# Optimization experiments

Measured on AMD Instinct MI355X. Metric: run time of the kernel, lower is better.

Reference implementation:

```python
import jax, jax.numpy as jnp
import numpy as np

DIM = 384
NUM_HEADS = 12
WINDOW = (8, 8)
HEAD_DIM = DIM // NUM_HEADS
CPB_HIDDEN = 512
MAX_LOGIT = float(np.log(1.0 / 0.01))  # clamp for logit_scale


def _relative_coords_table(ws):
    # log-spaced continuous relative coordinate table (Swin V2 style), ND
    axes = [np.arange(-(w - 1), w, dtype=np.float32) for w in ws]
    grid = np.stack(np.meshgrid(*axes, indexing='ij'), axis=-1)
    grid = grid.reshape(-1, len(ws))  # (prod(2w-1), nd)
    for i, w in enumerate(ws):
        grid[:, i] /= max(w - 1, 1)
    grid *= 8.0
    grid = np.sign(grid) * np.log2(np.abs(grid) + 1.0) / np.log2(8.0)
    return grid.astype(np.float32)


def _relative_position_index(ws):
    coords = np.stack(np.meshgrid(*[np.arange(w) for w in ws], indexing='ij'), axis=0)
    coords = coords.reshape(len(ws), -1)  # (nd, N)
    rel = coords[:, :, None] - coords[:, None, :]  # (nd, N, N)
    rel = rel.transpose(1, 2, 0).astype(np.int64)  # (N, N, nd)
    for i, w in enumerate(ws):
        rel[..., i] += w - 1
    # row-major strides over table dims of size (2w-1)
    stride = 1
    for i in range(len(ws) - 1, -1, -1):
        rel[..., i] *= stride
        stride *= 2 * ws[i] - 1
    return rel.sum(-1).astype(np.int32)  # (N, N)


def setup_inputs() -> dict:
    key = jax.random.key(0)
    ks = jax.random.split(key, 8)
    B, N = 1024, int(np.prod(WINDOW))
    x = jax.random.normal(ks[0], (B, N, DIM), dtype=jnp.float32)
    mask = jax.random.normal(ks[1], (64, N, N), dtype=jnp.float32)
    qkv_w = jax.random.normal(ks[2], (DIM, 3 * DIM), dtype=jnp.float32) * (DIM ** -0.5)
    proj_w = jax.random.normal(ks[3], (DIM, DIM), dtype=jnp.float32) * (DIM ** -0.5)
    proj_b = jnp.zeros((DIM,), dtype=jnp.float32)
    cpb_w1 = jax.random.normal(ks[4], (len(WINDOW), CPB_HIDDEN), dtype=jnp.float32) * 0.5
    cpb_b1 = jnp.zeros((CPB_HIDDEN,), dtype=jnp.float32)
    cpb_w2 = jax.random.normal(ks[5], (CPB_HIDDEN, NUM_HEADS), dtype=jnp.float32) * (CPB_HIDDEN ** -0.5)
    cpb_b2 = jnp.zeros((NUM_HEADS,), dtype=jnp.float32)
    logit_scale = jnp.log(jnp.ones((NUM_HEADS, 1, 1), dtype=jnp.float32) * 10.0)
    rpb_table = jnp.asarray(_relative_coords_table(WINDOW))
    rpb_idx = jnp.asarray(_relative_position_index(WINDOW))
    return dict(x=x, mask=mask, qkv_w=qkv_w, proj_w=proj_w, proj_b=proj_b,
                cpb_w1=cpb_w1, cpb_b1=cpb_b1, cpb_w2=cpb_w2, cpb_b2=cpb_b2,
                logit_scale=logit_scale, rpb_table=rpb_table, rpb_idx=rpb_idx)


def reference(x, mask, qkv_w, proj_w, proj_b, cpb_w1, cpb_b1, cpb_w2, cpb_b2,
              logit_scale, rpb_table, rpb_idx):
    B, N, _ = x.shape
    qkv = (x @ qkv_w).reshape(B, N, 3, NUM_HEADS, HEAD_DIM)
    qkv = qkv.transpose(2, 0, 3, 1, 4)  # (3, B, H, N, D)
    q, k, v = qkv[0], qkv[1], qkv[2]

    def _normalize(t):
        norm_sq = jnp.sum(t * t, axis=-1, keepdims=True)
        return t * jax.lax.rsqrt(jnp.maximum(norm_sq, 1e-12))

    q = _normalize(q)
    k = _normalize(k)
    attn = jnp.einsum('bhqd,bhkd->bhqk', q, k)
    scale = jnp.exp(jnp.minimum(logit_scale, MAX_LOGIT))  # (H,1,1)
    attn = attn * scale

    # continuous relative position bias MLP: Dense(512)+relu -> Dense(H)
    rpb = jax.nn.relu(rpb_table @ cpb_w1 + cpb_b1) @ cpb_w2 + cpb_b2  # (T, H)
    rpb = jnp.take(rpb, rpb_idx.reshape(-1), axis=0).reshape(N, N, NUM_HEADS)
    rpb = jnp.transpose(rpb, (2, 0, 1))  # (H, N, N)
    attn = attn + 16.0 * jax.nn.sigmoid(rpb)[None]

    n_w = mask.shape[0]
    attn = attn.reshape(B // n_w, n_w, NUM_HEADS, N, N)
    attn = attn + mask[None, :, None, :, :]
    attn = attn.reshape(B, NUM_HEADS, N, N)

    attn = jax.nn.softmax(attn, axis=-1)
    out = jnp.einsum('bhqk,bhkd->bhqd', attn, v)
    out = out.transpose(0, 2, 1, 3).reshape(B, N, DIM)
    return out @ proj_w + proj_b
```

## Files before the change

### kernel.cpp

```cpp
#include <hip/hip_runtime.h>

typedef unsigned short u16;
typedef __attribute__((ext_vector_type(8))) short short8;
typedef __attribute__((ext_vector_type(4))) float f32x4;

#define MFMA16(a, b, c) __builtin_amdgcn_mfma_f32_16x16x32_bf16((a), (b), (c), 0, 0, 0)

#define OFF_BIAS 0
#define OFF_SCALES 196608
#define OFF_RPB 196672
#define OFF_QKVF 207616
#define OFF_PROJF 1092352
#define OFF_XF 1387264
#define WS_NEED (1387264UL + 50331648UL)


__device__ __forceinline__ u16 f2bf(float f) {
  unsigned x = __float_as_uint(f);
  return (u16)((x + 0x7fffu + ((x >> 16) & 1u)) >> 16);
}

__global__ __launch_bounds__(256) void prep_cpb(const float* __restrict__ tab, const float* __restrict__ w1,
                                                const float* __restrict__ b1, const float* __restrict__ w2,
                                                const float* __restrict__ b2, float* __restrict__ rpb) {
  const int t = blockIdx.x;
  const int tid = threadIdx.x;
  const float t0 = tab[2 * t], t1 = tab[2 * t + 1];
  float acc[12];
#pragma unroll
  for (int h = 0; h < 12; ++h) acc[h] = 0.f;
  for (int j = tid; j < 512; j += 256) {
    const float hv = fmaxf(t0 * w1[j] + t1 * w1[512 + j] + b1[j], 0.f);
#pragma unroll
    for (int h = 0; h < 12; ++h) acc[h] += hv * w2[j * 12 + h];
  }
#pragma unroll
  for (int h = 0; h < 12; ++h)
#pragma unroll
    for (int off = 1; off < 64; off <<= 1) acc[h] += __shfl_xor(acc[h], off);
  __shared__ float red[4][12];
  const int wave = tid >> 6;
  if ((tid & 63) == 0) {
#pragma unroll
    for (int h = 0; h < 12; ++h) red[wave][h] = acc[h];
  }
  __syncthreads();
  if (tid < 12) rpb[t * 12 + tid] = red[0][tid] + red[1][tid] + red[2][tid] + red[3][tid] + b2[tid];
}

__global__ __launch_bounds__(256) void prep_all(const float* __restrict__ x,
                                                const float* __restrict__ qkv_w,
                                                const float* __restrict__ proj_w,
                                                const float* __restrict__ logit_scale,
                                                const float* __restrict__ rpb,
                                                const int* __restrict__ rpb_idx,
                                                u16* __restrict__ xF, u16* __restrict__ qkvF,
                                                u16* __restrict__ projF, float* __restrict__ scales,
                                                float* __restrict__ bias, int bid0) {
  __shared__ __align__(16) u16 sm[24576];
  const int bid = blockIdx.x + bid0;
  const int tid = threadIdx.x;
  if (bid < 1024) {
    const float4* x4 = reinterpret_cast<const float4*>(x + (long)bid * 24576);
#pragma unroll
    for (int it = 0; it < 12; ++it) {
      const int c = it * 256 + tid;
      const float4 a = x4[2 * c];
      const float4 b = x4[2 * c + 1];
      short8 v;
      v[0] = (short)f2bf(a.x); v[1] = (short)f2bf(a.y); v[2] = (short)f2bf(a.z); v[3] = (short)f2bf(a.w);
      v[4] = (short)f2bf(b.x); v[5] = (short)f2bf(b.y); v[6] = (short)f2bf(b.z); v[7] = (short)f2bf(b.w);
      const int row = c / 48;
      *reinterpret_cast<short8*>(sm + ((c * 8) ^ ((row & 7) << 3))) = v;
    }
    __syncthreads();
    u16* dst = xF + (long)bid * 24576;
#pragma unroll
    for (int it = 0; it < 12; ++it) {
      const int slot = it * 256 + tid;
      const int f = slot >> 6, l = slot & 63;
      const int row = 16 * (f & 3) + (l & 15);
      const int k0 = (f >> 2) * 32 + (l >> 4) * 8;
      const short8 v = *reinterpret_cast<const short8*>(sm + ((row * 384 + k0) ^ ((row & 7) << 3)));
      *reinterpret_cast<short8*>(dst + slot * 8) = v;
    }
  } else if (bid < 1168) {
    u16(*tile)[66] = reinterpret_cast<u16(*)[66]>(sm);
    const float* src;
    int W, rt, ct;
    const bool isqkv = bid < 1132;
    if (isqkv) {
      const int b = bid - 1024;
      src = qkv_w; W = 1152; rt = b / 18; ct = b % 18;
    } else {
      const int b = bid - 1132;
      src = proj_w; W = 384; rt = b / 6; ct = b % 6;
    }
#pragma unroll
    for (int kk = 0; kk < 4; ++kk) {
      const int idx = tid + kk * 256;
      const int r = idx >> 4, c4 = idx & 15;
      const float4 v = *reinterpret_cast<const float4*>(src + (long)(rt * 64 + r) * W + ct * 64 + c4 * 4);
      tile[r][c4 * 4 + 0] = f2bf(v.x);
      tile[r][c4 * 4 + 1] = f2bf(v.y);
      tile[r][c4 * 4 + 2] = f2bf(v.z);
      tile[r][c4 * 4 + 3] = f2bf(v.w);
    }
    __syncthreads();
#pragma unroll
    for (int kk = 0; kk < 4; ++kk) {
      const int idx = tid + kk * 256;
      const int c = idx >> 4, r0 = (idx & 15) * 4;
      ushort4 o;
      o.x = tile[r0 + 0][c];
      o.y = tile[r0 + 1][c];
      o.z = tile[r0 + 2][c];
      o.w = tile[r0 + 3][c];
      const int col = ct * 64 + c, k = rt * 64 + r0;
      const int lane = ((k >> 3) & 3) * 16 + (col & 15);
      const int e = k & 7;
      long off;
      if (isqkv) {
        const int m = col / 384, colm = col - m * 384;
        const int h = colm >> 5, jn = (colm >> 4) & 1;
        off = (long)(((h * 3 + m) * 24) + (k >> 5) * 2 + jn) * 512 + lane * 8 + e;
        *reinterpret_cast<ushort4*>(qkvF + off) = o;
      } else {
        const int w = col / 96, colw = col - w * 96;
        const int jn = colw >> 4;
        off = (long)(w * 72 + (k >> 5) * 6 + jn) * 512 + lane * 8 + e;
        *reinterpret_cast<ushort4*>(projF + off) = o;
      }
    }
  } else if (bid == 1168) {
    if (tid < 12) scales[tid] = __expf(fminf(logit_scale[tid], 4.6051702f));
  } else {
    const int p = (bid - 1169) * 256 + tid;
    const int t = rpb_idx[p];
#pragma unroll
    for (int h = 0; h < 12; ++h) bias[h * 4096 + p] = 16.f / (1.f + __expf(-rpb[t * 12 + h]));
  }
}

__global__ __launch_bounds__(768) void attn_fused(const u16* __restrict__ xF,
                                                  const float* __restrict__ mask,
                                                  const u16* __restrict__ qkvF,
                                                  const float* __restrict__ scales,
                                                  const float* __restrict__ bias,
                                                  const u16* __restrict__ projF,
                                                  const float* __restrict__ proj_b,
                                                  float* __restrict__ out) {
  __shared__ __align__(16) u16 sm[73728];
  const int tid = threadIdx.x;
  const int wave = tid >> 6, lane = tid & 63;
  const int q16 = lane >> 4, c16 = lane & 15;
  const int widx = blockIdx.x, wm = widx & 63;
  const int h = wave;
  u16* qs = sm + wave * 6144;
  u16* ks = qs + 2048;
  u16* ps = qs;
  u16* vst = qs + 4096;
  const u16* xw = xF + (long)widx * 24576;
  const u16* hb = qkvF + (long)h * 72 * 512;
  const float sc = scales[h];
  const f32x4 fzero = {0.f, 0.f, 0.f, 0.f};

  {
    f32x4 qa[4][2], ka[4][2];
#pragma unroll
    for (int i = 0; i < 4; ++i)
#pragma unroll
      for (int j = 0; j < 2; ++j) {
        qa[i][j] = fzero; ka[i][j] = fzero;
      }
#pragma unroll 1
    for (int t = 0; t < 12; ++t) {
      short8 af[4];
#pragma unroll
      for (int i = 0; i < 4; ++i)
        af[i] = *reinterpret_cast<const short8*>(xw + ((t * 4 + i) * 64 + lane) * 8);
#pragma unroll
      for (int jn = 0; jn < 2; ++jn) {
        const int fi = (2 * t + jn) * 512 + lane * 8;
        const short8 bq = *reinterpret_cast<const short8*>(hb + fi);
        const short8 bk = *reinterpret_cast<const short8*>(hb + 24 * 512 + fi);
#pragma unroll
        for (int i = 0; i < 4; ++i) {
          qa[i][jn] = MFMA16(af[i], bq, qa[i][jn]);
          ka[i][jn] = MFMA16(af[i], bk, ka[i][jn]);
        }
      }
    }
#pragma unroll
    for (int i = 0; i < 4; ++i) {
#pragma unroll
      for (int r = 0; r < 4; ++r) {
        const int row = 16 * i + 4 * q16 + r;
        float sq = qa[i][0][r] * qa[i][0][r] + qa[i][1][r] * qa[i][1][r];
        float sk = ka[i][0][r] * ka[i][0][r] + ka[i][1][r] * ka[i][1][r];
#pragma unroll
        for (int off = 1; off < 16; off <<= 1) {
          sq += __shfl_xor(sq, off);
          sk += __shfl_xor(sk, off);
        }
        const float rq = rsqrtf(fmaxf(sq, 1e-12f)) * sc;
        const float rk = rsqrtf(fmaxf(sk, 1e-12f));
        const int swq = (row & 3) << 3;
#pragma unroll
        for (int jn = 0; jn < 2; ++jn) {
          const int col = 16 * jn + c16;
          qs[(row * 32 + col) ^ swq] = f2bf(qa[i][jn][r] * rq);
          ks[(row * 32 + col) ^ swq] = f2bf(ka[i][jn][r] * rk);
        }
      }
    }
  }
  __builtin_amdgcn_sched_barrier(0);
  {
    f32x4 va[4][2];
#pragma unroll
    for (int i = 0; i < 4; ++i) {
      va[i][0] = fzero;
      va[i][1] = fzero;
    }
#pragma unroll 1
    for (int t = 0; t < 12; ++t) {
      short8 af[4];
#pragma unroll
      for (int i = 0; i < 4; ++i)
        af[i] = *reinterpret_cast<const short8*>(xw + ((t * 4 + i) * 64 + lane) * 8);
#pragma unroll
      for (int jn = 0; jn < 2; ++jn) {
        const short8 bv = *reinterpret_cast<const short8*>(hb + 48 * 512 + (2 * t + jn) * 512 + lane * 8);
#pragma unroll
        for (int i = 0; i < 4; ++i) va[i][jn] = MFMA16(af[i], bv, va[i][jn]);
      }
    }
#pragma unroll
    for (int i = 0; i < 4; ++i)
#pragma unroll
      for (int jn = 0; jn < 2; ++jn) {
        const int d = 16 * jn + c16;
        ushort4 vv;
        vv.x = f2bf(va[i][jn][0]);
        vv.y = f2bf(va[i][jn][1]);
        vv.z = f2bf(va[i][jn][2]);
        vv.w = f2bf(va[i][jn][3]);
        *reinterpret_cast<ushort4*>(vst + ((d * 64 + 16 * i + 4 * q16) ^ ((d & 7) << 3))) = vv;
      }
  }
  __builtin_amdgcn_sched_barrier(0);
  short8 aq[4], bk4[4];
#pragma unroll
  for (int i = 0; i < 4; ++i) {
    const int row = c16 + 16 * i;
    aq[i] = *reinterpret_cast<const short8*>(qs + ((row * 32 + q16 * 8) ^ ((row & 3) << 3)));
    bk4[i] = *reinterpret_cast<const short8*>(ks + ((row * 32 + q16 * 8) ^ ((row & 3) << 3)));
  }
  __builtin_amdgcn_sched_barrier(0);
  const float* bh = bias + h * 4096;
  const float* mw = mask + (long)wm * 4096;
#pragma unroll
  for (int i = 0; i < 4; ++i) {
    f32x4 si[4];
#pragma unroll
    for (int j = 0; j < 4; ++j) {
      const int col = 16 * j + c16;
#pragma unroll
      for (int r = 0; r < 4; ++r) {
        const int row = 16 * i + 4 * q16 + r;
        si[j][r] = bh[row * 64 + col] + mw[row * 64 + col];
      }
    }
#pragma unroll
    for (int j = 0; j < 4; ++j) si[j] = MFMA16(aq[i], bk4[j], si[j]);
#pragma unroll
    for (int r = 0; r < 4; ++r) {
      float m = fmaxf(fmaxf(si[0][r], si[1][r]), fmaxf(si[2][r], si[3][r]));
#pragma unroll
      for (int off = 1; off < 16; off <<= 1) m = fmaxf(m, __shfl_xor(m, off));
      float e[4], s = 0.f;
#pragma unroll
      for (int j = 0; j < 4; ++j) {
        e[j] = __expf(si[j][r] - m);
        s += e[j];
      }
#pragma unroll
      for (int off = 1; off < 16; off <<= 1) s += __shfl_xor(s, off);
      const float inv = 1.f / s;
      const int row = 16 * i + 4 * q16 + r;
      const int sw = (row & 7) << 3;
#pragma unroll
      for (int j = 0; j < 4; ++j) ps[(row * 64 + 16 * j + c16) ^ sw] = f2bf(e[j] * inv);
    }
    f32x4 oi[2];
    oi[0] = fzero;
    oi[1] = fzero;
    const int rowp = c16 + 16 * i;
#pragma unroll
    for (int kt = 0; kt < 2; ++kt) {
      const short8 api = *reinterpret_cast<const short8*>(
          ps + ((rowp * 64 + kt * 32 + q16 * 8) ^ ((rowp & 7) << 3)));
#pragma unroll
      for (int jn = 0; jn < 2; ++jn) {
        const int d = 16 * jn + c16;
        const short8 bvf = *reinterpret_cast<const short8*>(
            vst + ((d * 64 + kt * 32 + q16 * 8) ^ ((d & 7) << 3)));
        oi[jn] = MFMA16(api, bvf, oi[jn]);
      }
    }
#pragma unroll
    for (int jn = 0; jn < 2; ++jn)
#pragma unroll
      for (int r = 0; r < 4; ++r) {
        const int row = 16 * i + 4 * q16 + r;
        qs[(row * 32 + 16 * jn + c16) ^ ((row & 3) << 3)] = f2bf(oi[jn][r]);
      }
    __builtin_amdgcn_sched_barrier(0);
  }
  __syncthreads();
  const int n16a = wave * 2, n16b = wave * 2 + 1;
  const u16* pba = projF + (long)((n16a / 6) * 72 + (n16a % 6)) * 512;
  const u16* pbb = projF + (long)((n16b / 6) * 72 + (n16b % 6)) * 512;
  f32x4 pacc[4][2];
#pragma unroll
  for (int i = 0; i < 4; ++i) {
    pacc[i][0] = fzero;
    pacc[i][1] = fzero;
  }
#pragma unroll 1
  for (int t = 0; t < 12; ++t) {
    const u16* reg = sm + t * 6144;
    short8 af[4];
#pragma unroll
    for (int i = 0; i < 4; ++i) {
      const int row = c16 + 16 * i;
      af[i] = *reinterpret_cast<const short8*>(reg + ((row * 32 + q16 * 8) ^ ((row & 3) << 3)));
    }
    const short8 bwa = *reinterpret_cast<const short8*>(pba + (long)t * 6 * 512 + lane * 8);
    const short8 bwb = *reinterpret_cast<const short8*>(pbb + (long)t * 6 * 512 + lane * 8);
#pragma unroll
    for (int i = 0; i < 4; ++i) {
      pacc[i][0] = MFMA16(af[i], bwa, pacc[i][0]);
      pacc[i][1] = MFMA16(af[i], bwb, pacc[i][1]);
    }
  }
  float* ob = out + (long)widx * 24576;
#pragma unroll
  for (int jnp = 0; jnp < 2; ++jnp) {
    const int n = (wave * 2 + jnp) * 16 + c16;
    const float bv = proj_b[n];
#pragma unroll
    for (int i = 0; i < 4; ++i)
#pragma unroll
      for (int r = 0; r < 4; ++r)
        ob[(long)(16 * i + 4 * q16 + r) * 384 + n] = pacc[i][jnp][r] + bv;
  }
}

__global__ __launch_bounds__(256, 1) void attn_fb(const float* __restrict__ x,
                                                  const float* __restrict__ mask,
                                                  const u16* __restrict__ qkvF,
                                                  const float* __restrict__ scales,
                                                  const float* __restrict__ bias,
                                                  const u16* __restrict__ projF,
                                                  const float* __restrict__ proj_b,
                                                  float* __restrict__ out) {
  __shared__ __align__(16) u16 sm[49152];
  const int tid = threadIdx.x;
  const int wave = tid >> 6, lane = tid & 63;
  const int q16 = lane >> 4, c16 = lane & 15;
  const int widx = blockIdx.x, wm = widx & 63;
  u16* qs = sm + wave * 6144;
  u16* ks = qs + 2048;
  u16* ps = qs;
  u16* vst = qs + 4096;
  u16* xs = sm + 24576;
  const f32x4 fzero = {0.f, 0.f, 0.f, 0.f};
  {
    const float4* x4 = reinterpret_cast<const float4*>(x + (long)widx * 24576);
#pragma unroll
    for (int it = 0; it < 12; ++it) {
      const int c = it * 256 + tid;
      const float4 a = x4[2 * c];
      const float4 b = x4[2 * c + 1];
      short8 v;
      v[0] = (short)f2bf(a.x); v[1] = (short)f2bf(a.y); v[2] = (short)f2bf(a.z); v[3] = (short)f2bf(a.w);
      v[4] = (short)f2bf(b.x); v[5] = (short)f2bf(b.y); v[6] = (short)f2bf(b.z); v[7] = (short)f2bf(b.w);
      const int row = c / 48;
      *reinterpret_cast<short8*>(xs + ((c * 8) ^ ((row & 7) << 3))) = v;
    }
  }
  __syncthreads();
  unsigned ow[3][4][2][2];
#pragma unroll
  for (int hh = 0; hh < 3; ++hh) {
    const int h = wave * 3 + hh;
    const float sc = scales[h];
    const u16* hb = qkvF + (long)h * 72 * 512;
    f32x4 qa[4][2], ka[4][2], va[4][2];
#pragma unroll
    for (int i = 0; i < 4; ++i)
#pragma unroll
      for (int j = 0; j < 2; ++j) {
        qa[i][j] = fzero; ka[i][j] = fzero; va[i][j] = fzero;
      }
#pragma unroll 1
    for (int t = 0; t < 12; ++t) {
      const int k0 = t * 32 + q16 * 8;
      short8 af[4];
#pragma unroll
      for (int i = 0; i < 4; ++i) {
        const int row = c16 + 16 * i;
        af[i] = *reinterpret_cast<const short8*>(xs + ((row * 384 + k0) ^ ((row & 7) << 3)));
      }
#pragma unroll
      for (int jn = 0; jn < 2; ++jn) {
        const int fi = (2 * t + jn) * 512 + lane * 8;
        const short8 bq = *reinterpret_cast<const short8*>(hb + fi);
        const short8 bk = *reinterpret_cast<const short8*>(hb + 24 * 512 + fi);
        const short8 bv = *reinterpret_cast<const short8*>(hb + 48 * 512 + fi);
#pragma unroll
        for (int i = 0; i < 4; ++i) {
          qa[i][jn] = MFMA16(af[i], bq, qa[i][jn]);
          ka[i][jn] = MFMA16(af[i], bk, ka[i][jn]);
          va[i][jn] = MFMA16(af[i], bv, va[i][jn]);
        }
      }
    }
#pragma unroll
    for (int i = 0; i < 4; ++i) {
#pragma unroll
      for (int r = 0; r < 4; ++r) {
        const int row = 16 * i + 4 * q16 + r;
        float sq = qa[i][0][r] * qa[i][0][r] + qa[i][1][r] * qa[i][1][r];
        float sk = ka[i][0][r] * ka[i][0][r] + ka[i][1][r] * ka[i][1][r];
#pragma unroll
        for (int off = 1; off < 16; off <<= 1) {
          sq += __shfl_xor(sq, off);
          sk += __shfl_xor(sk, off);
        }
        const float rq = rsqrtf(fmaxf(sq, 1e-12f)) * sc;
        const float rk = rsqrtf(fmaxf(sk, 1e-12f));
        const int swq = (row & 3) << 3;
#pragma unroll
        for (int jn = 0; jn < 2; ++jn) {
          const int col = 16 * jn + c16;
          qs[(row * 32 + col) ^ swq] = f2bf(qa[i][jn][r] * rq);
          ks[(row * 32 + col) ^ swq] = f2bf(ka[i][jn][r] * rk);
          vst[(col * 64 + row) ^ ((col & 7) << 3)] = f2bf(va[i][jn][r]);
        }
      }
    }
    f32x4 sacc[4][4];
    {
      const float* bh = bias + h * 4096;
      const float* mw = mask + (long)wm * 4096;
#pragma unroll
      for (int i = 0; i < 4; ++i)
#pragma unroll
        for (int j = 0; j < 4; ++j) {
          const int col = 16 * j + c16;
#pragma unroll
          for (int r = 0; r < 4; ++r) {
            const int row = 16 * i + 4 * q16 + r;
            sacc[i][j][r] = bh[row * 64 + col] + mw[row * 64 + col];
          }
        }
    }
    short8 aq[4], bk4[4];
#pragma unroll
    for (int i = 0; i < 4; ++i) {
      const int row = c16 + 16 * i;
      aq[i] = *reinterpret_cast<const short8*>(qs + ((row * 32 + q16 * 8) ^ ((row & 3) << 3)));
      bk4[i] = *reinterpret_cast<const short8*>(ks + ((row * 32 + q16 * 8) ^ ((row & 3) << 3)));
    }
#pragma unroll
    for (int i = 0; i < 4; ++i)
#pragma unroll
      for (int j = 0; j < 4; ++j) sacc[i][j] = MFMA16(aq[i], bk4[j], sacc[i][j]);
#pragma unroll
    for (int i = 0; i < 4; ++i) {
#pragma unroll
      for (int r = 0; r < 4; ++r) {
        float m = fmaxf(fmaxf(sacc[i][0][r], sacc[i][1][r]), fmaxf(sacc[i][2][r], sacc[i][3][r]));
#pragma unroll
        for (int off = 1; off < 16; off <<= 1) m = fmaxf(m, __shfl_xor(m, off));
        float e[4], s = 0.f;
#pragma unroll
        for (int j = 0; j < 4; ++j) {
          e[j] = __expf(sacc[i][j][r] - m);
          s += e[j];
        }
#pragma unroll
        for (int off = 1; off < 16; off <<= 1) s += __shfl_xor(s, off);
        const float inv = 1.f / s;
        const int row = 16 * i + 4 * q16 + r;
        const int sw = (row & 7) << 3;
#pragma unroll
        for (int j = 0; j < 4; ++j) ps[(row * 64 + 16 * j + c16) ^ sw] = f2bf(e[j] * inv);
      }
    }
    f32x4 oa[4][2];
#pragma unroll
    for (int i = 0; i < 4; ++i) {
      oa[i][0] = fzero;
      oa[i][1] = fzero;
    }
#pragma unroll
    for (int kt = 0; kt < 2; ++kt) {
      short8 ap[4], bv2[2];
#pragma unroll
      for (int i = 0; i < 4; ++i) {
        const int row = c16 + 16 * i;
        ap[i] = *reinterpret_cast<const short8*>(ps + ((row * 64 + kt * 32 + q16 * 8) ^ ((row & 7) << 3)));
      }
#pragma unroll
      for (int jn = 0; jn < 2; ++jn) {
        const int d = 16 * jn + c16;
        bv2[jn] = *reinterpret_cast<const short8*>(vst + ((d * 64 + kt * 32 + q16 * 8) ^ ((d & 7) << 3)));
      }
#pragma unroll
      for (int i = 0; i < 4; ++i)
#pragma unroll
        for (int jn = 0; jn < 2; ++jn) oa[i][jn] = MFMA16(ap[i], bv2[jn], oa[i][jn]);
    }
#pragma unroll
    for (int i = 0; i < 4; ++i)
#pragma unroll
      for (int jn = 0; jn < 2; ++jn) {
        ow[hh][i][jn][0] = (unsigned)f2bf(oa[i][jn][0]) | ((unsigned)f2bf(oa[i][jn][1]) << 16);
        ow[hh][i][jn][1] = (unsigned)f2bf(oa[i][jn][2]) | ((unsigned)f2bf(oa[i][jn][3]) << 16);
      }
  }
  __syncthreads();
#pragma unroll
  for (int hh = 0; hh < 3; ++hh) {
    const int cb = (wave * 3 + hh) * 32;
#pragma unroll
    for (int i = 0; i < 4; ++i)
#pragma unroll
      for (int jn = 0; jn < 2; ++jn)
#pragma unroll
        for (int p = 0; p < 2; ++p) {
          const unsigned w = ow[hh][i][jn][p];
          const int col = cb + 16 * jn + c16;
          const int r0 = 16 * i + 4 * q16 + 2 * p;
          xs[(r0 * 384 + col) ^ ((r0 & 7) << 3)] = (u16)(w & 0xffffu);
          xs[((r0 + 1) * 384 + col) ^ (((r0 + 1) & 7) << 3)] = (u16)(w >> 16);
        }
  }
  __syncthreads();
  const u16* pb = projF + (long)wave * 72 * 512;
  f32x4 pacc[4][6];
#pragma unroll
  for (int i = 0; i < 4; ++i)
#pragma unroll
    for (int jn = 0; jn < 6; ++jn) pacc[i][jn] = fzero;
#pragma unroll 1
  for (int t = 0; t < 12; ++t) {
    const int k0 = t * 32 + q16 * 8;
    short8 af[4];
#pragma unroll
    for (int i = 0; i < 4; ++i) {
      const int row = c16 + 16 * i;
      af[i] = *reinterpret_cast<const short8*>(xs + ((row * 384 + k0) ^ ((row & 7) << 3)));
    }
#pragma unroll
    for (int jn = 0; jn < 6; ++jn) {
      const short8 bw = *reinterpret_cast<const short8*>(pb + (t * 6 + jn) * 512 + lane * 8);
#pragma unroll
      for (int i = 0; i < 4; ++i) pacc[i][jn] = MFMA16(af[i], bw, pacc[i][jn]);
    }
  }
  float* ob = out + (long)widx * 24576;
#pragma unroll
  for (int jn = 0; jn < 6; ++jn) {
    const int n = wave * 96 + 16 * jn + c16;
    const float bv = proj_b[n];
#pragma unroll
    for (int i = 0; i < 4; ++i)
#pragma unroll
      for (int r = 0; r < 4; ++r)
        ob[(long)(16 * i + 4 * q16 + r) * 384 + n] = pacc[i][jn][r] + bv;
  }
}

extern "C" void kernel_launch(void* const* d_in, const int* in_sizes, int n_in, void* d_out,
                              int out_size, void* d_ws, size_t ws_size, hipStream_t stream) {
  const float* x = (const float*)d_in[0];
  const float* mask = (const float*)d_in[1];
  const float* qkv_w = (const float*)d_in[2];
  const float* proj_w = (const float*)d_in[3];
  const float* proj_b = (const float*)d_in[4];
  const float* cpb_w1 = (const float*)d_in[5];
  const float* cpb_b1 = (const float*)d_in[6];
  const float* cpb_w2 = (const float*)d_in[7];
  const float* cpb_b2 = (const float*)d_in[8];
  const float* logit_scale = (const float*)d_in[9];
  const float* rpb_table = (const float*)d_in[10];
  const int* rpb_idx = (const int*)d_in[11];

  char* ws = (char*)d_ws;
  float* bias = (float*)(ws + OFF_BIAS);
  float* scales = (float*)(ws + OFF_SCALES);
  float* rpb = (float*)(ws + OFF_RPB);
  u16* qkvF = (u16*)(ws + OFF_QKVF);
  u16* projF = (u16*)(ws + OFF_PROJF);
  u16* xF = (u16*)(ws + OFF_XF);

  prep_cpb<<<225, 256, 0, stream>>>(rpb_table, cpb_w1, cpb_b1, cpb_w2, cpb_b2, rpb);
  const bool big = ws_size >= WS_NEED;
  if (big) {
    prep_all<<<1185, 256, 0, stream>>>(x, qkv_w, proj_w, logit_scale, rpb, rpb_idx,
                                       xF, qkvF, projF, scales, bias, 0);
    attn_fused<<<1024, 768, 0, stream>>>(xF, mask, qkvF, scales, bias, projF, proj_b,
                                         (float*)d_out);
  } else {
    prep_all<<<161, 256, 0, stream>>>(x, qkv_w, proj_w, logit_scale, rpb, rpb_idx,
                                      xF, qkvF, projF, scales, bias, 1024);
    attn_fb<<<1024, 256, 0, stream>>>(x, mask, qkvF, scales, bias, projF, proj_b, (float*)d_out);
  }
}
```

Baseline: 343.7 us.

## Fuse CPB MLP into prep kernel and gather sigmoid bias in attention

Removes the separate prep_cpb launch by folding the per-table-entry position-bias MLP into extra blocks of prep_all, which now stores the 16*sigmoid bias per table entry (225x12) instead of a full 12x64x64 expanded bias. The attention kernels gather the bias through rpb_idx at use time. This saves one launch and the expanded bias write, at the cost of an indirect, dependent load per score element. The fallback attention kernel is also rewritten to use 768 threads with one head per wave, matching the fused path.

```diff
diff --git a/kernel.cpp b/kernel.cpp
--- a/kernel.cpp
+++ b/kernel.cpp
@@ -6,9 +6,8 @@
 
 #define MFMA16(a, b, c) __builtin_amdgcn_mfma_f32_16x16x32_bf16((a), (b), (c), 0, 0, 0)
 
-#define OFF_BIAS 0
-#define OFF_SCALES 196608
-#define OFF_RPB 196672
+#define OFF_SIG 0
+#define OFF_SCALES 16384
 #define OFF_QKVF 207616
 #define OFF_PROJF 1092352
 #define OFF_XF 1387264
@@ -20,43 +19,18 @@
   return (u16)((x + 0x7fffu + ((x >> 16) & 1u)) >> 16);
 }
 
-__global__ __launch_bounds__(256) void prep_cpb(const float* __restrict__ tab, const float* __restrict__ w1,
-                                                const float* __restrict__ b1, const float* __restrict__ w2,
-                                                const float* __restrict__ b2, float* __restrict__ rpb) {
-  const int t = blockIdx.x;
-  const int tid = threadIdx.x;
-  const float t0 = tab[2 * t], t1 = tab[2 * t + 1];
-  float acc[12];
-#pragma unroll
-  for (int h = 0; h < 12; ++h) acc[h] = 0.f;
-  for (int j = tid; j < 512; j += 256) {
-    const float hv = fmaxf(t0 * w1[j] + t1 * w1[512 + j] + b1[j], 0.f);
-#pragma unroll
-    for (int h = 0; h < 12; ++h) acc[h] += hv * w2[j * 12 + h];
-  }
-#pragma unroll
-  for (int h = 0; h < 12; ++h)
-#pragma unroll
-    for (int off = 1; off < 64; off <<= 1) acc[h] += __shfl_xor(acc[h], off);
-  __shared__ float red[4][12];
-  const int wave = tid >> 6;
-  if ((tid & 63) == 0) {
-#pragma unroll
-    for (int h = 0; h < 12; ++h) red[wave][h] = acc[h];
-  }
-  __syncthreads();
-  if (tid < 12) rpb[t * 12 + tid] = red[0][tid] + red[1][tid] + red[2][tid] + red[3][tid] + b2[tid];
-}
-
 __global__ __launch_bounds__(256) void prep_all(const float* __restrict__ x,
                                                 const float* __restrict__ qkv_w,
                                                 const float* __restrict__ proj_w,
                                                 const float* __restrict__ logit_scale,
-                                                const float* __restrict__ rpb,
-                                                const int* __restrict__ rpb_idx,
+                                                const float* __restrict__ tab,
+                                                const float* __restrict__ w1,
+                                                const float* __restrict__ b1,
+                                                const float* __restrict__ w2,
+                                                const float* __restrict__ b2,
                                                 u16* __restrict__ xF, u16* __restrict__ qkvF,
                                                 u16* __restrict__ projF, float* __restrict__ scales,
-                                                float* __restrict__ bias, int bid0) {
+                                                float* __restrict__ sig, int bid0) {
   __shared__ __align__(16) u16 sm[24576];
   const int bid = blockIdx.x + bid0;
   const int tid = threadIdx.x;
@@ -135,10 +109,31 @@
   } else if (bid == 1168) {
     if (tid < 12) scales[tid] = __expf(fminf(logit_scale[tid], 4.6051702f));
   } else {
-    const int p = (bid - 1169) * 256 + tid;
-    const int t = rpb_idx[p];
-#pragma unroll
-    for (int h = 0; h < 12; ++h) bias[h * 4096 + p] = 16.f / (1.f + __expf(-rpb[t * 12 + h]));
+    const int t = bid - 1169;
+    const float t0 = tab[2 * t], t1 = tab[2 * t + 1];
+    float acc[12];
+#pragma unroll
+    for (int h = 0; h < 12; ++h) acc[h] = 0.f;
+    for (int j = tid; j < 512; j += 256) {
+      const float hv = fmaxf(t0 * w1[j] + t1 * w1[512 + j] + b1[j], 0.f);
+#pragma unroll
+      for (int h = 0; h < 12; ++h) acc[h] += hv * w2[j * 12 + h];
+    }
+#pragma unroll
+    for (int h = 0; h < 12; ++h)
+#pragma unroll
+      for (int off = 1; off < 64; off <<= 1) acc[h] += __shfl_xor(acc[h], off);
+    float* red = reinterpret_cast<float*>(sm);
+    const int wave = tid >> 6;
+    if ((tid & 63) == 0) {
+#pragma unroll
+      for (int h = 0; h < 12; ++h) red[wave * 12 + h] = acc[h];
+    }
+    __syncthreads();
+    if (tid < 12) {
+      const float v = red[tid] + red[12 + tid] + red[24 + tid] + red[36 + tid] + b2[tid];
+      sig[t * 12 + tid] = 16.f / (1.f + __expf(-v));
+    }
   }
 }
 
@@ -146,7 +141,8 @@
                                                   const float* __restrict__ mask,
                                                   const u16* __restrict__ qkvF,
                                                   const float* __restrict__ scales,
-                                                  const float* __restrict__ bias,
+                                                  const int* __restrict__ rpb_idx,
+                                                  const float* __restrict__ sig,
                                                   const u16* __restrict__ projF,
                                                   const float* __restrict__ proj_b,
                                                   float* __restrict__ out) {
@@ -258,7 +254,6 @@
     bk4[i] = *reinterpret_cast<const short8*>(ks + ((row * 32 + q16 * 8) ^ ((row & 3) << 3)));
   }
   __builtin_amdgcn_sched_barrier(0);
-  const float* bh = bias + h * 4096;
   const float* mw = mask + (long)wm * 4096;
 #pragma unroll
   for (int i = 0; i < 4; ++i) {
@@ -269,7 +264,8 @@
 #pragma unroll
       for (int r = 0; r < 4; ++r) {
         const int row = 16 * i + 4 * q16 + r;
-        si[j][r] = bh[row * 64 + col] + mw[row * 64 + col];
+        const int p = row * 64 + col;
+        si[j][r] = sig[rpb_idx[p] * 12 + h] + mw[p];
       }
     }
 #pragma unroll
@@ -358,73 +354,69 @@
   }
 }
 
-__global__ __launch_bounds__(256, 1) void attn_fb(const float* __restrict__ x,
-                                                  const float* __restrict__ mask,
-                                                  const u16* __restrict__ qkvF,
-                                                  const float* __restrict__ scales,
-                                                  const float* __restrict__ bias,
-                                                  const u16* __restrict__ projF,
-                                                  const float* __restrict__ proj_b,
-                                                  float* __restrict__ out) {
-  __shared__ __align__(16) u16 sm[49152];
+__global__ __launch_bounds__(768) void attn_fb(const float* __restrict__ x,
+                                               const float* __restrict__ mask,
+                                               const u16* __restrict__ qkvF,
+                                               const float* __restrict__ scales,
+                                               const int* __restrict__ rpb_idx,
+                                               const float* __restrict__ sig,
+                                               const u16* __restrict__ projF,
+                                               const float* __restrict__ proj_b,
+                                               float* __restrict__ out) {
+  __shared__ __align__(16) u16 sm[73728];
+  u16* xs = sm;
   const int tid = threadIdx.x;
   const int wave = tid >> 6, lane = tid & 63;
   const int q16 = lane >> 4, c16 = lane & 15;
   const int widx = blockIdx.x, wm = widx & 63;
-  u16* qs = sm + wave * 6144;
-  u16* ks = qs + 2048;
-  u16* ps = qs;
-  u16* vst = qs + 4096;
-  u16* xs = sm + 24576;
-  const f32x4 fzero = {0.f, 0.f, 0.f, 0.f};
+  const int h = wave;
   {
-    const float4* x4 = reinterpret_cast<const float4*>(x + (long)widx * 24576);
-#pragma unroll
-    for (int it = 0; it < 12; ++it) {
-      const int c = it * 256 + tid;
-      const float4 a = x4[2 * c];
-      const float4 b = x4[2 * c + 1];
+    const float* xwf = x + (long)widx * 24576;
+#pragma unroll
+    for (int it = 0; it < 4; ++it) {
+      const int slot = it * 768 + tid;
+      const int f = slot >> 6, l = slot & 63;
+      const int row = 16 * (f & 3) + (l & 15);
+      const int k0 = (f >> 2) * 32 + (l >> 4) * 8;
+      const float4 a = *reinterpret_cast<const float4*>(xwf + row * 384 + k0);
+      const float4 b = *reinterpret_cast<const float4*>(xwf + row * 384 + k0 + 4);
       short8 v;
       v[0] = (short)f2bf(a.x); v[1] = (short)f2bf(a.y); v[2] = (short)f2bf(a.z); v[3] = (short)f2bf(a.w);
       v[4] = (short)f2bf(b.x); v[5] = (short)f2bf(b.y); v[6] = (short)f2bf(b.z); v[7] = (short)f2bf(b.w);
-      const int row = c / 48;
-      *reinterpret_cast<short8*>(xs + ((c * 8) ^ ((row & 7) << 3))) = v;
+      *reinterpret_cast<short8*>(xs + slot * 8) = v;
     }
   }
   __syncthreads();
-  unsigned ow[3][4][2][2];
-#pragma unroll
-  for (int hh = 0; hh < 3; ++hh) {
-    const int h = wave * 3 + hh;
-    const float sc = scales[h];
-    const u16* hb = qkvF + (long)h * 72 * 512;
-    f32x4 qa[4][2], ka[4][2], va[4][2];
+  u16* qs = sm + 24576 + wave * 4096;
+  u16* ks = qs + 2048;
+  u16* ps = qs;
+  const u16* hb = qkvF + (long)h * 72 * 512;
+  const float sc = scales[h];
+  const f32x4 fzero = {0.f, 0.f, 0.f, 0.f};
+  f32x4 va[4][2];
+  {
+    f32x4 qa[4][2], ka[4][2];
 #pragma unroll
     for (int i = 0; i < 4; ++i)
 #pragma unroll
       for (int j = 0; j < 2; ++j) {
-        qa[i][j] = fzero; ka[i][j] = fzero; va[i][j] = fzero;
+        qa[i][j] = fzero; ka[i][j] = fzero;
       }
 #pragma unroll 1
     for (int t = 0; t < 12; ++t) {
-      const int k0 = t * 32 + q16 * 8;
       short8 af[4];
 #pragma unroll
-      for (int i = 0; i < 4; ++i) {
-        const int row = c16 + 16 * i;
-        af[i] = *reinterpret_cast<const short8*>(xs + ((row * 384 + k0) ^ ((row & 7) << 3)));
-      }
+      for (int i = 0; i < 4; ++i)
+        af[i] = *reinterpret_cast<const short8*>(xs + ((t * 4 + i) * 64 + lane) * 8);
 #pragma unroll
       for (int jn = 0; jn < 2; ++jn) {
         const int fi = (2 * t + jn) * 512 + lane * 8;
         const short8 bq = *reinterpret_cast<const short8*>(hb + fi);
         const short8 bk = *reinterpret_cast<const short8*>(hb + 24 * 512 + fi);
-        const short8 bv = *reinterpret_cast<const short8*>(hb + 48 * 512 + fi);
 #pragma unroll
         for (int i = 0; i < 4; ++i) {
           qa[i][jn] = MFMA16(af[i], bq, qa[i][jn]);
           ka[i][jn] = MFMA16(af[i], bk, ka[i][jn]);
-          va[i][jn] = MFMA16(af[i], bv, va[i][jn]);
         }
       }
     }
@@ -448,141 +440,160 @@
           const int col = 16 * jn + c16;
           qs[(row * 32 + col) ^ swq] = f2bf(qa[i][jn][r] * rq);
           ks[(row * 32 + col) ^ swq] = f2bf(ka[i][jn][r] * rk);
-          vst[(col * 64 + row) ^ ((col & 7) << 3)] = f2bf(va[i][jn][r]);
         }
       }
     }
-    f32x4 sacc[4][4];
-    {
-      const float* bh = bias + h * 4096;
-      const float* mw = mask + (long)wm * 4096;
-#pragma unroll
-      for (int i = 0; i < 4; ++i)
-#pragma unroll
-        for (int j = 0; j < 4; ++j) {
-          const int col = 16 * j + c16;
-#pragma unroll
-          for (int r = 0; r < 4; ++r) {
-            const int row = 16 * i + 4 * q16 + r;
-            sacc[i][j][r] = bh[row * 64 + col] + mw[row * 64 + col];
-          }
-        }
-    }
-    short8 aq[4], bk4[4];
-#pragma unroll
-    for (int i = 0; i < 4; ++i) {
-      const int row = c16 + 16 * i;
-      aq[i] = *reinterpret_cast<const short8*>(qs + ((row * 32 + q16 * 8) ^ ((row & 3) << 3)));
-      bk4[i] = *reinterpret_cast<const short8*>(ks + ((row * 32 + q16 * 8) ^ ((row & 3) << 3)));
-    }
-#pragma unroll
-    for (int i = 0; i < 4; ++i)
-#pragma unroll
-      for (int j = 0; j < 4; ++j) sacc[i][j] = MFMA16(aq[i], bk4[j], sacc[i][j]);
-#pragma unroll
-    for (int i = 0; i < 4; ++i) {
-#pragma unroll
-      for (int r = 0; r < 4; ++r) {
-        float m = fmaxf(fmaxf(sacc[i][0][r], sacc[i][1][r]), fmaxf(sacc[i][2][r], sacc[i][3][r]));
-#pragma unroll
-        for (int off = 1; off < 16; off <<= 1) m = fmaxf(m, __shfl_xor(m, off));
-        float e[4], s = 0.f;
-#pragma unroll
-        for (int j = 0; j < 4; ++j) {
-          e[j] = __expf(sacc[i][j][r] - m);
-          s += e[j];
-        }
-#pragma unroll
-        for (int off = 1; off < 16; off <<= 1) s += __shfl_xor(s, off);
-        const float inv = 1.f / s;
-        const int row = 16 * i + 4 * q16 + r;
-        const int sw = (row & 7) << 3;
-#pragma unroll
-        for (int j = 0; j < 4; ++j) ps[(row * 64 + 16 * j + c16) ^ sw] = f2bf(e[j] * inv);
-      }
-    }
-    f32x4 oa[4][2];
-#pragma unroll
-    for (int i = 0; i < 4; ++i) {
-      oa[i][0] = fzero;
-      oa[i][1] = fzero;
-    }
-#pragma unroll
-    for (int kt = 0; kt < 2; ++kt) {
-      short8 ap[4], bv2[2];
-#pragma unroll
-      for (int i = 0; i < 4; ++i) {
-        const int row = c16 + 16 * i;
-        ap[i] = *reinterpret_cast<const short8*>(ps + ((row * 64 + kt * 32 + q16 * 8) ^ ((row & 7) << 3)));
-      }
-#pragma unroll
-      for (int jn = 0; jn < 2; ++jn) {
-        const int d = 16 * jn + c16;
-        bv2[jn] = *reinterpret_cast<const short8*>(vst + ((d * 64 + kt * 32 + q16 * 8) ^ ((d & 7) << 3)));
-      }
-#pragma unroll
-      for (int i = 0; i < 4; ++i)
-#pragma unroll
-        for (int jn = 0; jn < 2; ++jn) oa[i][jn] = MFMA16(ap[i], bv2[jn], oa[i][jn]);
-    }
-#pragma unroll
-    for (int i = 0; i < 4; ++i)
-#pragma unroll
-      for (int jn = 0; jn < 2; ++jn) {
-        ow[hh][i][jn][0] = (unsigned)f2bf(oa[i][jn][0]) | ((unsigned)f2bf(oa[i][jn][1]) << 16);
-        ow[hh][i][jn][1] = (unsigned)f2bf(oa[i][jn][2]) | ((unsigned)f2bf(oa[i][jn][3]) << 16);
-      }
-  }
-  __syncthreads();
-#pragma unroll
-  for (int hh = 0; hh < 3; ++hh) {
-    const int cb = (wave * 3 + hh) * 32;
-#pragma unroll
-    for (int i = 0; i < 4; ++i)
-#pragma unroll
-      for (int jn = 0; jn < 2; ++jn)
-#pragma unroll
-        for (int p = 0; p < 2; ++p) {
-          const unsigned w = ow[hh][i][jn][p];
-          const int col = cb + 16 * jn + c16;
-          const int r0 = 16 * i + 4 * q16 + 2 * p;
-          xs[(r0 * 384 + col) ^ ((r0 & 7) << 3)] = (u16)(w & 0xffffu);
-          xs[((r0 + 1) * 384 + col) ^ (((r0 + 1) & 7) << 3)] = (u16)(w >> 16);
-        }
-  }
-  __syncthreads();
-  const u16* pb = projF + (long)wave * 72 * 512;
-  f32x4 pacc[4][6];
-#pragma unroll
-  for (int i = 0; i < 4; ++i)
-#pragma unroll
-    for (int jn = 0; jn < 6; ++jn) pacc[i][jn] = fzero;
+  }
+#pragma unroll
+  for (int i = 0; i < 4; ++i) {
+    va[i][0] = fzero;
+    va[i][1] = fzero;
+  }
 #pragma unroll 1
   for (int t = 0; t < 12; ++t) {
-    const int k0 = t * 32 + q16 * 8;
     short8 af[4];
 #pragma unroll
+    for (int i = 0; i < 4; ++i)
+      af[i] = *reinterpret_cast<const short8*>(xs + ((t * 4 + i) * 64 + lane) * 8);
+#pragma unroll
+    for (int jn = 0; jn < 2; ++jn) {
+      const short8 bv = *reinterpret_cast<const short8*>(hb + 48 * 512 + (2 * t + jn) * 512 + lane * 8);
+#pragma unroll
+      for (int i = 0; i < 4; ++i) va[i][jn] = MFMA16(af[i], bv, va[i][jn]);
+    }
+  }
+  short8 aq[4], bk4[4];
+#pragma unroll
+  for (int i = 0; i < 4; ++i) {
+    const int row = c16 + 16 * i;
+    aq[i] = *reinterpret_cast<const short8*>(qs + ((row * 32 + q16 * 8) ^ ((row & 3) << 3)));
+    bk4[i] = *reinterpret_cast<const short8*>(ks + ((row * 32 + q16 * 8) ^ ((row & 3) << 3)));
+  }
+  const float* mw = mask + (long)wm * 4096;
+  f32x4 sacc[4][4];
+#pragma unroll
+  for (int i = 0; i < 4; ++i)
+#pragma unroll
+    for (int j = 0; j < 4; ++j) {
+      const int col = 16 * j + c16;
+#pragma unroll
+      for (int r = 0; r < 4; ++r) {
+        const int p = (16 * i + 4 * q16 + r) * 64 + col;
+        sacc[i][j][r] = sig[rpb_idx[p] * 12 + h] + mw[p];
+      }
+    }
+#pragma unroll
+  for (int i = 0; i < 4; ++i)
+#pragma unroll
+    for (int j = 0; j < 4; ++j) sacc[i][j] = MFMA16(aq[i], bk4[j], sacc[i][j]);
+#pragma unroll
+  for (int i = 0; i < 4; ++i)
+#pragma unroll
+    for (int r = 0; r < 4; ++r) {
+      float m = fmaxf(fmaxf(sacc[i][0][r], sacc[i][1][r]), fmaxf(sacc[i][2][r], sacc[i][3][r]));
+#pragma unroll
+      for (int off = 1; off < 16; off <<= 1) m = fmaxf(m, __shfl_xor(m, off));
+      float e[4], s = 0.f;
+#pragma unroll
+      for (int j = 0; j < 4; ++j) {
+        e[j] = __expf(sacc[i][j][r] - m);
+        s += e[j];
+      }
+#pragma unroll
+      for (int off = 1; off < 16; off <<= 1) s += __shfl_xor(s, off);
+      const float inv = 1.f / s;
+      const int row = 16 * i + 4 * q16 + r;
+      const int sw = (row & 7) << 3;
+#pragma unroll
+      for (int j = 0; j < 4; ++j) ps[(row * 64 + 16 * j + c16) ^ sw] = f2bf(e[j] * inv);
+    }
+  __syncthreads();
+  u16* vstb = sm + wave * 4096;
+#pragma unroll
+  for (int i = 0; i < 4; ++i)
+#pragma unroll
+    for (int jn = 0; jn < 2; ++jn) {
+      const int d = 16 * jn + c16;
+      ushort4 vv;
+      vv.x = f2bf(va[i][jn][0]);
+      vv.y = f2bf(va[i][jn][1]);
+      vv.z = f2bf(va[i][jn][2]);
+      vv.w = f2bf(va[i][jn][3]);
+      *reinterpret_cast<ushort4*>(vstb + ((d * 64 + 16 * i + 4 * q16) ^ ((d & 7) << 3))) = vv;
+    }
+  f32x4 oa[4][2];
+#pragma unroll
+  for (int i = 0; i < 4; ++i) {
+    oa[i][0] = fzero;
+    oa[i][1] = fzero;
+  }
+#pragma unroll
+  for (int kt = 0; kt < 2; ++kt) {
+    short8 ap[4], bv2[2];
+#pragma unroll
     for (int i = 0; i < 4; ++i) {
       const int row = c16 + 16 * i;
-      af[i] = *reinterpret_cast<const short8*>(xs + ((row * 384 + k0) ^ ((row & 7) << 3)));
-    }
-#pragma unroll
-    for (int jn = 0; jn < 6; ++jn) {
-      const short8 bw = *reinterpret_cast<const short8*>(pb + (t * 6 + jn) * 512 + lane * 8);
-#pragma unroll
-      for (int i = 0; i < 4; ++i) pacc[i][jn] = MFMA16(af[i], bw, pacc[i][jn]);
+      ap[i] = *reinterpret_cast<const short8*>(ps + ((row * 64 + kt * 32 + q16 * 8) ^ ((row & 7) << 3)));
+    }
+#pragma unroll
+    for (int jn = 0; jn < 2; ++jn) {
+      const int d = 16 * jn + c16;
+      bv2[jn] = *reinterpret_cast<const short8*>(vstb + ((d * 64 + kt * 32 + q16 * 8) ^ ((d & 7) << 3)));
+    }
+#pragma unroll
+    for (int i = 0; i < 4; ++i)
+#pragma unroll
+      for (int jn = 0; jn < 2; ++jn) oa[i][jn] = MFMA16(ap[i], bv2[jn], oa[i][jn]);
+  }
+  __syncthreads();
+  u16* ot = sm + 24576 + wave * 2048;
+  ot = sm + wave * 4096;
+#pragma unroll
+  for (int i = 0; i < 4; ++i)
+#pragma unroll
+    for (int jn = 0; jn < 2; ++jn)
+#pragma unroll
+      for (int r = 0; r < 4; ++r) {
+        const int row = 16 * i + 4 * q16 + r;
+        ot[(row * 32 + 16 * jn + c16) ^ ((row & 3) << 3)] = f2bf(oa[i][jn][r]);
+      }
+  __syncthreads();
+  const int n16a = wave * 2, n16b = wave * 2 + 1;
+  const u16* pba = projF + (long)((n16a / 6) * 72 + (n16a % 6)) * 512;
+  const u16* pbb = projF + (long)((n16b / 6) * 72 + (n16b % 6)) * 512;
+  f32x4 pacc[4][2];
+#pragma unroll
+  for (int i = 0; i < 4; ++i) {
+    pacc[i][0] = fzero;
+    pacc[i][1] = fzero;
+  }
+#pragma unroll 1
+  for (int t = 0; t < 12; ++t) {
+    const u16* reg = sm + t * 4096;
+    short8 af[4];
+#pragma unroll
+    for (int i = 0; i < 4; ++i) {
+      const int row = c16 + 16 * i;
+      af[i] = *reinterpret_cast<const short8*>(reg + ((row * 32 + q16 * 8) ^ ((row & 3) << 3)));
+    }
+    const short8 bwa = *reinterpret_cast<const short8*>(pba + (long)t * 6 * 512 + lane * 8);
+    const short8 bwb = *reinterpret_cast<const short8*>(pbb + (long)t * 6 * 512 + lane * 8);
+#pragma unroll
+    for (int i = 0; i < 4; ++i) {
+      pacc[i][0] = MFMA16(af[i], bwa, pacc[i][0]);
+      pacc[i][1] = MFMA16(af[i], bwb, pacc[i][1]);
     }
   }
   float* ob = out + (long)widx * 24576;
 #pragma unroll
-  for (int jn = 0; jn < 6; ++jn) {
-    const int n = wave * 96 + 16 * jn + c16;
+  for (int jnp = 0; jnp < 2; ++jnp) {
+    const int n = (wave * 2 + jnp) * 16 + c16;
     const float bv = proj_b[n];
 #pragma unroll
     for (int i = 0; i < 4; ++i)
 #pragma unroll
       for (int r = 0; r < 4; ++r)
-        ob[(long)(16 * i + 4 * q16 + r) * 384 + n] = pacc[i][jn][r] + bv;
+        ob[(long)(16 * i + 4 * q16 + r) * 384 + n] = pacc[i][jnp][r] + bv;
   }
 }
 
@@ -602,23 +613,22 @@
   const int* rpb_idx = (const int*)d_in[11];
 
   char* ws = (char*)d_ws;
-  float* bias = (float*)(ws + OFF_BIAS);
+  float* sig = (float*)(ws + OFF_SIG);
   float* scales = (float*)(ws + OFF_SCALES);
-  float* rpb = (float*)(ws + OFF_RPB);
   u16* qkvF = (u16*)(ws + OFF_QKVF);
   u16* projF = (u16*)(ws + OFF_PROJF);
   u16* xF = (u16*)(ws + OFF_XF);
 
-  prep_cpb<<<225, 256, 0, stream>>>(rpb_table, cpb_w1, cpb_b1, cpb_w2, cpb_b2, rpb);
   const bool big = ws_size >= WS_NEED;
   if (big) {
-    prep_all<<<1185, 256, 0, stream>>>(x, qkv_w, proj_w, logit_scale, rpb, rpb_idx,
-                                       xF, qkvF, projF, scales, bias, 0);
-    attn_fused<<<1024, 768, 0, stream>>>(xF, mask, qkvF, scales, bias, projF, proj_b,
+    prep_all<<<1394, 256, 0, stream>>>(x, qkv_w, proj_w, logit_scale, rpb_table, cpb_w1,
+                                       cpb_b1, cpb_w2, cpb_b2, xF, qkvF, projF, scales, sig, 0);
+    attn_fused<<<1024, 768, 0, stream>>>(xF, mask, qkvF, scales, rpb_idx, sig, projF, proj_b,
                                          (float*)d_out);
   } else {
-    prep_all<<<161, 256, 0, stream>>>(x, qkv_w, proj_w, logit_scale, rpb, rpb_idx,
-                                      xF, qkvF, projF, scales, bias, 1024);
-    attn_fb<<<1024, 256, 0, stream>>>(x, mask, qkvF, scales, bias, projF, proj_b, (float*)d_out);
+    prep_all<<<370, 256, 0, stream>>>(x, qkv_w, proj_w, logit_scale, rpb_table, cpb_w1,
+                                      cpb_b1, cpb_w2, cpb_b2, xF, qkvF, projF, scales, sig, 1024);
+    attn_fb<<<1024, 768, 0, stream>>>(x, mask, qkvF, scales, rpb_idx, sig, projF, proj_b,
+                                      (float*)d_out);
   }
 }
```

Result: slower. 361.1 us (+5.0%).
